# Kernel optimization log

Measured on AMD Instinct MI355X. Metric: run time of the kernel, lower is better.

Reference implementation:

```python
import jax, jax.numpy as jnp
import numpy as np

N, DZ, L, H, MLPH, INC = 256, 256, 256, 512, 2048, 8
CAT_IDX = np.arange(0, 192, 2)                      # 96 categorical token positions (interleaved)
NUM_IDX = np.setdiff1d(np.arange(L), CAT_IDX)       # 160 numerical token positions
CARDS = [4, 16, 128]                                # cardinality per categorical group
GSZ = 32                                            # tokens per categorical group
NUM_CARD = 100                                      # cardinality of quantized numerical params


def setup_inputs() -> dict:
    ks = list(jax.random.split(jax.random.key(0), 24))
    def nrm(shape, s=0.02):
        return jax.random.normal(ks.pop(), shape, jnp.float32) * s
    inp = {}
    inp['z'] = jax.random.normal(ks.pop(), (N, DZ), jnp.float32)
    inp['mlp_w0'] = nrm((DZ, MLPH)); inp['mlp_b0'] = jnp.zeros((MLPH,), jnp.float32)
    inp['mlp_w1'] = nrm((MLPH, MLPH)); inp['mlp_b1'] = jnp.zeros((MLPH,), jnp.float32)
    inp['mlp_w2'] = nrm((MLPH, MLPH)); inp['mlp_b2'] = jnp.zeros((MLPH,), jnp.float32)
    inp['conv_w'] = nrm((H, INC)); inp['conv_b'] = jnp.zeros((H,), jnp.float32)
    for g, card in enumerate(CARDS):
        inp[f'cat_w{g}'] = nrm((H, card)); inp[f'cat_b{g}'] = jnp.zeros((card,), jnp.float32)
    inp['num_w'] = nrm((H, 2)); inp['num_b'] = jnp.zeros((2,), jnp.float32)
    inp['num_target'] = jax.random.uniform(ks.pop(), (N, len(NUM_IDX)), jnp.float32)
    inp['cat_target'] = jax.random.randint(ks.pop(), (N, len(CAT_IDX)), 0, 4, jnp.int32)
    return inp


def reference(z, mlp_w0, mlp_b0, mlp_w1, mlp_b1, mlp_w2, mlp_b2, conv_w, conv_b,
              cat_w0, cat_b0, cat_w1, cat_b1, cat_w2, cat_b2, num_w, num_b,
              num_target, cat_target):
    n = z.shape[0]
    # MLP: fc0 -> act -> fc1 -> act -> fc2
    h = z @ mlp_w0 + mlp_b0
    h = jax.nn.relu(h) @ mlp_w1 + mlp_b1
    h = jax.nn.relu(h) @ mlp_w2 + mlp_b2
    h = h.reshape(n, INC, L)                        # (N, C=8, L)
    # act + 1x1 conv to hidden_size, then transpose -> (N, L, H)
    u = jnp.einsum('ncl,hc->nlh', jax.nn.relu(h), conv_w) + conv_b
    # ---- categorical tokens: gather, per-cardinality heads, CE NLL, argmax sample ----
    hc = u[:, CAT_IDX, :]                           # (N, 96, H)
    heads = [(cat_w0, cat_b0), (cat_w1, cat_b1), (cat_w2, cat_b2)]
    nlls, samps = [], []
    for g, (w, b) in enumerate(heads):
        hg = hc[:, g * GSZ:(g + 1) * GSZ, :]        # (N, 32, H)
        logits = hg @ w + b                         # (N, 32, card)
        logp = jax.nn.log_softmax(logits, axis=-1)
        tg = cat_target[:, g * GSZ:(g + 1) * GSZ]
        nlls.append(-jnp.take_along_axis(logp, tg[..., None], axis=-1)[..., 0])
        samps.append(jnp.argmax(logits, axis=-1))
    cat_nll = jnp.concatenate(nlls, axis=1)         # (N, 96)
    cat_samples = jnp.concatenate(samps, axis=1)    # (N, 96)
    # ---- numerical tokens: gather, 2-param discretized logistic, NLL, mode sample ----
    hn = u[:, NUM_IDX, :]                           # (N, 160, H)
    p = hn @ num_w + num_b                          # (N, 160, 2)
    mu = jax.nn.sigmoid(p[..., 0])
    s = jax.nn.softplus(p[..., 1]) + 1e-4
    hb = 1.0 / (2.0 * (NUM_CARD - 1))               # half bin width
    t = num_target
    cdf_p = jax.nn.sigmoid((t + hb - mu) / s)
    cdf_m = jax.nn.sigmoid((t - hb - mu) / s)
    prob = jnp.where(t < hb, cdf_p, jnp.where(t > 1.0 - hb, 1.0 - cdf_m, cdf_p - cdf_m))
    num_nll = -jnp.log(jnp.maximum(prob, 1e-7))     # (N, 160)
    num_samples = jax.lax.stop_gradient(jnp.round(mu * (NUM_CARD - 1)) / (NUM_CARD - 1))
    # ---- scatter samples back into the preallocated output tensor ----
    u_out = jnp.zeros((n, L, 3), jnp.float32)
    u_out = u_out.at[:, CAT_IDX, 0].set(cat_samples.astype(jnp.float32))
    u_out = u_out.at[:, NUM_IDX, 1].set(num_samples)
    return u_out, cat_nll, num_nll
```

## Files before the change

### kernel.cpp

```cpp
#include <hip/hip_runtime.h>
#include <hip/hip_fp16.h>
#include <math.h>

#define NN   256
#define LL   256
#define HH   512
#define MLPHv 2048
#define INCv 8
#define NCOLS 150

typedef _Float16 f16x8 __attribute__((ext_vector_type(8)));
typedef float    f32x4 __attribute__((ext_vector_type(4)));
typedef unsigned short ushort_t;

__device__ __forceinline__ void split1(float f, ushort_t& h, ushort_t& l)
{
    __half hh = __float2half_rn(f);
    h = __half_as_ushort(hh);
    l = __half_as_ushort(__float2half_rn((f - __half2float(hh)) * 4096.f));
}

__device__ __forceinline__ void pack8(const float* fv, uint4& hv, uint4& lv)
{
    ushort_t h[8], l[8];
#pragma unroll
    for (int j = 0; j < 8; ++j) split1(fv[j], h[j], l[j]);
    hv.x = (unsigned)h[0] | ((unsigned)h[1] << 16);
    hv.y = (unsigned)h[2] | ((unsigned)h[3] << 16);
    hv.z = (unsigned)h[4] | ((unsigned)h[5] << 16);
    hv.w = (unsigned)h[6] | ((unsigned)h[7] << 16);
    lv.x = (unsigned)l[0] | ((unsigned)l[1] << 16);
    lv.y = (unsigned)l[2] | ((unsigned)l[3] << 16);
    lv.z = (unsigned)l[4] | ((unsigned)l[5] << 16);
    lv.w = (unsigned)l[6] | ((unsigned)l[7] << 16);
}

typedef __attribute__((address_space(3))) unsigned int lds_u32;
typedef __attribute__((address_space(1))) const unsigned int glb_u32;
__device__ __forceinline__ void gl_lds16(const ushort_t* g, ushort_t* l)
{
    __builtin_amdgcn_global_load_lds((glb_u32*)g, (lds_u32*)l, 16, 0, 0);
}


__global__ __launch_bounds__(256) void prep_all(
    const float* __restrict__ z,
    const float* __restrict__ w0, const float* __restrict__ w1,
    const float* __restrict__ w2,
    const float* __restrict__ cvw, const float* __restrict__ cvb,
    const float* __restrict__ cw0, const float* __restrict__ cb0,
    const float* __restrict__ cw1, const float* __restrict__ cb1,
    const float* __restrict__ cw2, const float* __restrict__ cb2,
    const float* __restrict__ nw,  const float* __restrict__ nbv,
    ushort_t* __restrict__ W0th, ushort_t* __restrict__ W0tl,
    ushort_t* __restrict__ W1th, ushort_t* __restrict__ W1tl,
    ushort_t* __restrict__ W2th, ushort_t* __restrict__ W2tl,
    ushort_t* __restrict__ zh, ushort_t* __restrict__ zl,
    float* __restrict__ Mf, float* __restrict__ beta)
{
    const int bid = blockIdx.x;
    const int tid = threadIdx.x;
    if (bid < 2176) {
        __shared__ float lfs[64 * 68];
        const float* src; ushort_t* dh; ushort_t* dl; int KS32v, t;
        if (bid < 1024)      { src = w1; dh = W1th; dl = W1tl; KS32v = 64; t = bid; }
        else if (bid < 2048) { src = w2; dh = W2th; dl = W2tl; KS32v = 64; t = bid - 1024; }
        else                 { src = w0; dh = W0th; dl = W0tl; KS32v = 8;  t = bid - 2048; }
        const int k0 = (t >> 5) * 64;
        const int n0 = (t & 31) * 64;
        {
            const int r  = tid >> 2;
            const int cb = (tid & 3) * 16;
            const float* p = src + (size_t)(k0 + r) * 2048 + n0 + cb;
#pragma unroll
            for (int q = 0; q < 4; ++q)
                *(float4*)&lfs[r * 68 + cb + q * 4] = *(const float4*)(p + q * 4);
        }
        __syncthreads();
        {
            const int c  = tid >> 2;
            const int kq = tid & 3;
            ushort_t hb[16], lb[16];
#pragma unroll
            for (int j = 0; j < 16; ++j)
                split1(lfs[(kq * 16 + j) * 68 + c], hb[j], lb[j]);
            const int gn  = (n0 + c) >> 4;
            const int l16 = c & 15;
#pragma unroll
            for (int o = 0; o < 2; ++o) {
                const int koct  = (k0 >> 3) + kq * 2 + o;
                const int ks    = koct >> 2, koct3 = koct & 3;
                const size_t off = ((size_t)(gn * KS32v + ks) * 64 + l16 + (koct3 << 4)) * 8;
                uint4 v;
                v.x = (unsigned)hb[o*8+0] | ((unsigned)hb[o*8+1] << 16);
                v.y = (unsigned)hb[o*8+2] | ((unsigned)hb[o*8+3] << 16);
                v.z = (unsigned)hb[o*8+4] | ((unsigned)hb[o*8+5] << 16);
                v.w = (unsigned)hb[o*8+6] | ((unsigned)hb[o*8+7] << 16);
                *(uint4*)&dh[off] = v;
                v.x = (unsigned)lb[o*8+0] | ((unsigned)lb[o*8+1] << 16);
                v.y = (unsigned)lb[o*8+2] | ((unsigned)lb[o*8+3] << 16);
                v.z = (unsigned)lb[o*8+4] | ((unsigned)lb[o*8+5] << 16);
                v.w = (unsigned)lb[o*8+6] | ((unsigned)lb[o*8+7] << 16);
                *(uint4*)&dl[off] = v;
            }
        }
    } else if (bid < 2192) {
        const int idx = (bid - 2176) * 256 + tid;
        const int r = idx >> 4, kq = idx & 15;
        const float* p = z + (size_t)r * 256 + kq * 16;
        float fv[16];
#pragma unroll
        for (int q = 0; q < 4; ++q) {
            float4 v = *(const float4*)(p + q * 4);
            fv[q * 4 + 0] = v.x; fv[q * 4 + 1] = v.y;
            fv[q * 4 + 2] = v.z; fv[q * 4 + 3] = v.w;
        }
        ushort_t hb[16], lb[16];
#pragma unroll
        for (int j = 0; j < 16; ++j) split1(fv[j], hb[j], lb[j]);
        const int gm = r >> 4, l16 = r & 15;
#pragma unroll
        for (int o = 0; o < 2; ++o) {
            const int koct = kq * 2 + o;
            const int ks = koct >> 2, koct3 = koct & 3;
            const size_t off = ((size_t)(gm * 8 + ks) * 64 + l16 + (koct3 << 4)) * 8;
            uint4 v;
            v.x = (unsigned)hb[o*8+0] | ((unsigned)hb[o*8+1] << 16);
            v.y = (unsigned)hb[o*8+2] | ((unsigned)hb[o*8+3] << 16);
            v.z = (unsigned)hb[o*8+4] | ((unsigned)hb[o*8+5] << 16);
            v.w = (unsigned)hb[o*8+6] | ((unsigned)hb[o*8+7] << 16);
            *(uint4*)&zh[off] = v;
            v.x = (unsigned)lb[o*8+0] | ((unsigned)lb[o*8+1] << 16);
            v.y = (unsigned)lb[o*8+2] | ((unsigned)lb[o*8+3] << 16);
            v.z = (unsigned)lb[o*8+4] | ((unsigned)lb[o*8+5] << 16);
            v.w = (unsigned)lb[o*8+6] | ((unsigned)lb[o*8+7] << 16);
            *(uint4*)&zl[off] = v;
        }
    } else {
        const int k = bid - 2192;
        const float* W; const float* B; int off, card;
        if (k < 4)        { W = cw0; B = cb0; off = 0;   card = 4;   }
        else if (k < 20)  { W = cw1; B = cb1; off = 4;   card = 16;  }
        else if (k < 148) { W = cw2; B = cb2; off = 20;  card = 128; }
        else              { W = nw;  B = nbv; off = 148; card = 2;   }
        const int kc = k - off;
        float part[INCv + 1];
#pragma unroll
        for (int c = 0; c <= INCv; ++c) part[c] = 0.f;
#pragma unroll
        for (int it = 0; it < 2; ++it) {
            const int h = tid + it * 256;
            const float wv = W[h * card + kc];
#pragma unroll
            for (int c = 0; c < INCv; ++c) part[c] += cvw[h * INCv + c] * wv;
            part[INCv] += cvb[h] * wv;
        }
        __shared__ float red[INCv + 1][4];
        const int lane = tid & 63, wave = tid >> 6;
#pragma unroll
        for (int c = 0; c <= INCv; ++c) {
            float v = part[c];
#pragma unroll
            for (int o = 32; o >= 1; o >>= 1) v += __shfl_down(v, o, 64);
            if (lane == 0) red[c][wave] = v;
        }
        __syncthreads();
        if (tid <= INCv) {
            const float s = red[tid][0] + red[tid][1] + red[tid][2] + red[tid][3];
            if (tid < INCv) Mf[tid * NCOLS + k] = s;
            else            beta[k] = s + B[kc];
        }
    }
}

template <int OUT>
__global__ __launch_bounds__(512, 4) void gemm_pk(
    const ushort_t* __restrict__ Ah, const ushort_t* __restrict__ Al,
    const ushort_t* __restrict__ Bh, const ushort_t* __restrict__ Bl,
    const float* __restrict__ bias, float* __restrict__ part,
    ushort_t* __restrict__ oH, ushort_t* __restrict__ oL,
    int KS32, int kchunk32, int steps)
{
    __shared__ ushort_t sAh[2][8192];
    __shared__ ushort_t sAl[2][8192];
    __shared__ ushort_t sBh[2][4096];
    __shared__ ushort_t sBl[2][4096];

    const int tid  = threadIdx.x;
    const int lane = tid & 63, w = tid >> 6;
    const int wr   = w >> 1, wc = w & 1;
    const int bx   = blockIdx.x, by = blockIdx.y, bz = blockIdx.z;
    const int kb0  = bz * kchunk32;

    f32x4 accH[2][2], accC[2][2];
#pragma unroll
    for (int r = 0; r < 2; ++r)
#pragma unroll
        for (int c = 0; c < 2; ++c) {
            accH[r][c] = (f32x4){0.f, 0.f, 0.f, 0.f};
            accC[r][c] = (f32x4){0.f, 0.f, 0.f, 0.f};
        }

    {
        const int kb = kb0;
#pragma unroll
        for (int i = 0; i < 2; ++i) {
            const int run = w + i * 8;
            const int g = run >> 1, ks = run & 1;
            const size_t f = ((size_t)(by * 8 + g) * KS32 + kb + ks) * 512 + lane * 8;
            gl_lds16(Ah + f, &sAh[0][run * 512]);
            gl_lds16(Al + f, &sAl[0][run * 512]);
        }
        const int g = w >> 1, ks = w & 1;
        const size_t f = ((size_t)(bx * 4 + g) * KS32 + kb + ks) * 512 + lane * 8;
        gl_lds16(Bh + f, &sBh[0][w * 512]);
        gl_lds16(Bl + f, &sBl[0][w * 512]);
    }

    for (int t = 0; t < steps; ++t) {
        const int cur = t & 1;
        const int nxt = t + 1;
        if (nxt < steps) {
            const int kb = kb0 + nxt * 2;
            const int nb = nxt & 1;
#pragma unroll
            for (int i = 0; i < 2; ++i) {
                const int run = w + i * 8;
                const int g = run >> 1, ks = run & 1;
                const size_t f = ((size_t)(by * 8 + g) * KS32 + kb + ks) * 512 + lane * 8;
                gl_lds16(Ah + f, &sAh[nb][run * 512]);
                gl_lds16(Al + f, &sAl[nb][run * 512]);
            }
            const int g = w >> 1, ks = w & 1;
            const size_t f = ((size_t)(bx * 4 + g) * KS32 + kb + ks) * 512 + lane * 8;
            gl_lds16(Bh + f, &sBh[nb][w * 512]);
            gl_lds16(Bl + f, &sBl[nb][w * 512]);
            asm volatile("s_waitcnt vmcnt(6)" ::: "memory");
        } else {
            asm volatile("s_waitcnt vmcnt(0)" ::: "memory");
        }
        __builtin_amdgcn_s_barrier();

#pragma unroll
        for (int ks = 0; ks < 2; ++ks) {
            f16x8 aH[2], aL[2], bHf[2], bLf[2];
#pragma unroll
            for (int r = 0; r < 2; ++r) {
                const int off = (((wr * 2 + r) * 2 + ks) * 64 + lane) * 8;
                aH[r] = *(const f16x8*)&sAh[cur][off];
                aL[r] = *(const f16x8*)&sAl[cur][off];
            }
#pragma unroll
            for (int c = 0; c < 2; ++c) {
                const int off = (((wc * 2 + c) * 2 + ks) * 64 + lane) * 8;
                bHf[c] = *(const f16x8*)&sBh[cur][off];
                bLf[c] = *(const f16x8*)&sBl[cur][off];
            }
#pragma unroll
            for (int r = 0; r < 2; ++r)
#pragma unroll
                for (int c = 0; c < 2; ++c) {
                    accH[r][c] = __builtin_amdgcn_mfma_f32_16x16x32_f16(aH[r], bHf[c], accH[r][c], 0, 0, 0);
                    accC[r][c] = __builtin_amdgcn_mfma_f32_16x16x32_f16(aH[r], bLf[c], accC[r][c], 0, 0, 0);
                    accC[r][c] = __builtin_amdgcn_mfma_f32_16x16x32_f16(aL[r], bHf[c], accC[r][c], 0, 0, 0);
                }
        }
        __builtin_amdgcn_s_barrier();
    }

    const float inv = 1.f / 4096.f;
#pragma unroll
    for (int r = 0; r < 2; ++r)
#pragma unroll
        for (int c = 0; c < 2; ++c) {
            const int row0 = by * 128 + (wr * 2 + r) * 16 + ((lane >> 4) << 2);
            const int col  = bx * 64  + (wc * 2 + c) * 16 + (lane & 15);
            if (OUT == 0) {
                float* po = part + (size_t)bz * 524288;
#pragma unroll
                for (int e = 0; e < 4; ++e)
                    po[(size_t)(row0 + e) * 2048 + col] = accH[r][c][e] + accC[r][c][e] * inv;
            } else {
                const float vb = bias[col];
                const int gm = (by * 8 + wr * 2 + r);
                const int ks = col >> 5, koct3 = (col >> 3) & 3, j = col & 7;
                const size_t fb = ((size_t)(gm * 64 + ks) * 64) * 8 + (koct3 << 4) * 8 + j;
#pragma unroll
                for (int e = 0; e < 4; ++e) {
                    const float v = fmaxf(accH[r][c][e] + accC[r][c][e] * inv + vb, 0.f);
                    ushort_t h, l;
                    split1(v, h, l);
                    const int l16 = ((lane >> 4) << 2) + e;
                    oH[fb + (size_t)l16 * 8] = h;
                    oL[fb + (size_t)l16 * 8] = l;
                }
            }
        }
}

__global__ __launch_bounds__(256) void reduce_pk(
    const float* __restrict__ part, const float* __restrict__ bias,
    ushort_t* __restrict__ oH, ushort_t* __restrict__ oL)
{
    const int b  = blockIdx.x;
    const int ct = b & 15, rg = b >> 4;
    const int e  = threadIdx.x * 4;
    const int row = rg * 8 + (e >> 7);
    const int col = ct * 128 + (e & 127);
    const size_t idx = (size_t)row * 2048 + col;
    float4 s = *(const float4*)&bias[col];
#pragma unroll
    for (int k = 0; k < 4; ++k) {
        const float4 p = *(const float4*)&part[(size_t)k * 524288 + idx];
        s.x += p.x; s.y += p.y; s.z += p.z; s.w += p.w;
    }
    s.x = fmaxf(s.x, 0.f); s.y = fmaxf(s.y, 0.f);
    s.z = fmaxf(s.z, 0.f); s.w = fmaxf(s.w, 0.f);
    ushort_t h[4], l[4];
    split1(s.x, h[0], l[0]); split1(s.y, h[1], l[1]);
    split1(s.z, h[2], l[2]); split1(s.w, h[3], l[3]);
    const int gm = row >> 4, l16 = row & 15;
    const int ks = col >> 5, koct3 = (col >> 3) & 3, j = col & 7;
    const size_t off = ((size_t)(gm * 64 + ks) * 64 + l16 + (koct3 << 4)) * 8 + j;
    ushort4 hv = {h[0], h[1], h[2], h[3]};
    ushort4 lv = {l[0], l[1], l[2], l[3]};
    *(ushort4*)&oH[off] = hv;
    *(ushort4*)&oL[off] = lv;
}

__global__ __launch_bounds__(256) void heads_kernel(
    const float* __restrict__ part, const float* __restrict__ b2,
    const float* __restrict__ Mf, const float* __restrict__ beta,
    const int* __restrict__ cat_target, const float* __restrict__ num_target,
    float* __restrict__ out)
{
    const int bx  = blockIdx.x;
    const int tid = threadIdx.x;
    __shared__ float Ms[INCv][128];
    __shared__ float Bsh[128];
    if (bx < 96) {
        const int g = bx >> 5;
        const int card = (g == 0) ? 4 : (g == 1) ? 16 : 128;
        const int off  = (g == 0) ? 0 : (g == 1) ? 4  : 20;
        for (int i = tid; i < card * INCv; i += 256) {
            int c = i / card, k = i % card;
            Ms[c][k] = Mf[c * NCOLS + off + k];
        }
        for (int i = tid; i < card; i += 256) Bsh[i] = beta[off + i];
        __syncthreads();

        const int idx = (bx & 31) * 256 + tid;
        const int n = idx >> 5, j = idx & 31;
        const int ci = g * 32 + j;
        const int l  = ci * 2;
        float rv[INCv];
#pragma unroll
        for (int c = 0; c < INCv; ++c) {
            const size_t e = (size_t)n * MLPHv + c * LL + l;
            float s = b2[c * LL + l];
#pragma unroll
            for (int k = 0; k < 4; ++k) s += part[(size_t)k * 524288 + e];
            rv[c] = fmaxf(s, 0.f);
        }

        float mx = -1e30f; int arg = 0;
        for (int k = 0; k < card; ++k) {
            float s = Bsh[k];
#pragma unroll
            for (int c = 0; c < INCv; ++c) s += rv[c] * Ms[c][k];
            if (s > mx) { mx = s; arg = k; }
        }
        const int tg = cat_target[n * 96 + ci];
        float sum = 0.f, stg = 0.f;
        for (int k = 0; k < card; ++k) {
            float s = Bsh[k];
#pragma unroll
            for (int c = 0; c < INCv; ++c) s += rv[c] * Ms[c][k];
            sum += expf(s - mx);
            if (k == tg) stg = s;
        }
        const float lse = mx + logf(sum);
        out[NN * LL * 3 + n * 96 + ci] = lse - stg;
        float* u = out + (size_t)(n * LL + l) * 3;
        u[0] = (float)arg; u[1] = 0.f; u[2] = 0.f;
    } else {
        const int idx = (bx - 96) * 256 + tid;
        const int n = idx / 160, ni = idx % 160;
        const int l = (ni < 96) ? (2 * ni + 1) : (96 + ni);
        float rv[INCv];
#pragma unroll
        for (int c = 0; c < INCv; ++c) {
            const size_t e = (size_t)n * MLPHv + c * LL + l;
            float s = b2[c * LL + l];
#pragma unroll
            for (int k = 0; k < 4; ++k) s += part[(size_t)k * 524288 + e];
            rv[c] = fmaxf(s, 0.f);
        }
        float p0 = beta[148], p1 = beta[149];
#pragma unroll
        for (int c = 0; c < INCv; ++c) {
            p0 += rv[c] * Mf[c * NCOLS + 148];
            p1 += rv[c] * Mf[c * NCOLS + 149];
        }
        const float mu = 1.f / (1.f + expf(-p0));
        const float sp = (p1 > 20.f) ? p1 : log1pf(expf(p1));
        const float s  = sp + 1e-4f;
        const float hb = 1.f / 198.f;
        const float t  = num_target[n * 160 + ni];
        const float cp = 1.f / (1.f + expf(-((t + hb - mu) / s)));
        const float cm = 1.f / (1.f + expf(-((t - hb - mu) / s)));
        const float prob = (t < hb) ? cp : ((t > 1.f - hb) ? (1.f - cm) : (cp - cm));
        out[NN * LL * 3 + NN * 96 + n * 160 + ni] = -logf(fmaxf(prob, 1e-7f));
        float* u = out + (size_t)(n * LL + l) * 3;
        u[0] = 0.f; u[1] = rintf(mu * 99.f) / 99.f; u[2] = 0.f;
    }
}

extern "C" void kernel_launch(void* const* d_in, const int* in_sizes, int n_in,
                              void* d_out, int out_size, void* d_ws, size_t ws_size,
                              hipStream_t stream)
{
    const float* z   = (const float*)d_in[0];
    const float* w0  = (const float*)d_in[1];
    const float* b0  = (const float*)d_in[2];
    const float* w1  = (const float*)d_in[3];
    const float* b1  = (const float*)d_in[4];
    const float* w2  = (const float*)d_in[5];
    const float* b2  = (const float*)d_in[6];
    const float* cvw = (const float*)d_in[7];
    const float* cvb = (const float*)d_in[8];
    const float* cw0 = (const float*)d_in[9];
    const float* cb0 = (const float*)d_in[10];
    const float* cw1 = (const float*)d_in[11];
    const float* cb1 = (const float*)d_in[12];
    const float* cw2 = (const float*)d_in[13];
    const float* cb2 = (const float*)d_in[14];
    const float* nw  = (const float*)d_in[15];
    const float* nb  = (const float*)d_in[16];
    const float* num_target = (const float*)d_in[17];
    const int*   cat_target = (const int*)d_in[18];
    float* out = (float*)d_out;
    float* ws  = (float*)d_ws;

    size_t o = 0;
    float*    part = ws + o;                o += 4ull * 524288;
    float*    Mf   = ws + o;                o += 1536;
    float*    beta = ws + o;                o += 256;
    ushort_t* zh   = (ushort_t*)(ws + o);   o += 32768;
    ushort_t* zl   = (ushort_t*)(ws + o);   o += 32768;
    ushort_t* r0h  = (ushort_t*)(ws + o);   o += 262144;
    ushort_t* r0l  = (ushort_t*)(ws + o);   o += 262144;
    ushort_t* r1h  = (ushort_t*)(ws + o);   o += 262144;
    ushort_t* r1l  = (ushort_t*)(ws + o);   o += 262144;
    ushort_t* W0th = (ushort_t*)(ws + o);   o += 262144;
    ushort_t* W0tl = (ushort_t*)(ws + o);   o += 262144;
    ushort_t* W1th = (ushort_t*)(ws + o);   o += 2097152;
    ushort_t* W1tl = (ushort_t*)(ws + o);   o += 2097152;
    ushort_t* W2th = (ushort_t*)(ws + o);   o += 2097152;
    ushort_t* W2tl = (ushort_t*)(ws + o);   o += 2097152;

    prep_all<<<dim3(2342), 256, 0, stream>>>(
        z, w0, w1, w2, cvw, cvb, cw0, cb0, cw1, cb1, cw2, cb2, nw, nb,
        W0th, W0tl, W1th, W1tl, W2th, W2tl, zh, zl, Mf, beta);

    gemm_pk<1><<<dim3(32, 2, 1), 512, 0, stream>>>(
        zh, zl, W0th, W0tl, b0, nullptr, r0h, r0l, 8, 8, 4);

    gemm_pk<0><<<dim3(32, 2, 4), 512, 0, stream>>>(
        r0h, r0l, W1th, W1tl, nullptr, part, nullptr, nullptr, 64, 16, 8);
    reduce_pk<<<dim3(512), 256, 0, stream>>>(part, b1, r1h, r1l);

    gemm_pk<0><<<dim3(32, 2, 4), 512, 0, stream>>>(
        r1h, r1l, W2th, W2tl, nullptr, part, nullptr, nullptr, 64, 16, 8);

    heads_kernel<<<dim3(256), 256, 0, stream>>>(
        part, b2, Mf, beta, cat_target, num_target, out);
}
```

Before: 77.81 us.

## Fuse weight fp16 hi/lo split into GEMM tile loads, drop prep pass

Removes the separate prep pass that converted and repacked the full fp32 MLP weights into fp16 hi/lo tiled buffers. Each GEMM block now loads raw fp32 weight tiles into LDS and splits and packs them to fp16 hi/lo in shared memory before the MFMA steps. This saves a full read-convert-write round trip over about 32 MB of weights. In exchange, each weight tile is converted once per M-block (twice here), each step gains an extra barrier, and LDS use grows, so launch bounds drop to one block per SM.

After: 73.73 us. 5.2% less time.

```diff
diff --git a/kernel.cpp b/kernel.cpp
--- a/kernel.cpp
+++ b/kernel.cpp
@@ -41,71 +41,26 @@
 {
     __builtin_amdgcn_global_load_lds((glb_u32*)g, (lds_u32*)l, 16, 0, 0);
 }
-
-
-__global__ __launch_bounds__(256) void prep_all(
+__device__ __forceinline__ void gl_lds16f(const float* g, float* l)
+{
+    __builtin_amdgcn_global_load_lds((glb_u32*)g, (lds_u32*)l, 16, 0, 0);
+}
+
+
+__global__ __launch_bounds__(256) void prep_small(
     const float* __restrict__ z,
-    const float* __restrict__ w0, const float* __restrict__ w1,
-    const float* __restrict__ w2,
     const float* __restrict__ cvw, const float* __restrict__ cvb,
     const float* __restrict__ cw0, const float* __restrict__ cb0,
     const float* __restrict__ cw1, const float* __restrict__ cb1,
     const float* __restrict__ cw2, const float* __restrict__ cb2,
     const float* __restrict__ nw,  const float* __restrict__ nbv,
-    ushort_t* __restrict__ W0th, ushort_t* __restrict__ W0tl,
-    ushort_t* __restrict__ W1th, ushort_t* __restrict__ W1tl,
-    ushort_t* __restrict__ W2th, ushort_t* __restrict__ W2tl,
     ushort_t* __restrict__ zh, ushort_t* __restrict__ zl,
     float* __restrict__ Mf, float* __restrict__ beta)
 {
     const int bid = blockIdx.x;
     const int tid = threadIdx.x;
-    if (bid < 2176) {
-        __shared__ float lfs[64 * 68];
-        const float* src; ushort_t* dh; ushort_t* dl; int KS32v, t;
-        if (bid < 1024)      { src = w1; dh = W1th; dl = W1tl; KS32v = 64; t = bid; }
-        else if (bid < 2048) { src = w2; dh = W2th; dl = W2tl; KS32v = 64; t = bid - 1024; }
-        else                 { src = w0; dh = W0th; dl = W0tl; KS32v = 8;  t = bid - 2048; }
-        const int k0 = (t >> 5) * 64;
-        const int n0 = (t & 31) * 64;
-        {
-            const int r  = tid >> 2;
-            const int cb = (tid & 3) * 16;
-            const float* p = src + (size_t)(k0 + r) * 2048 + n0 + cb;
-#pragma unroll
-            for (int q = 0; q < 4; ++q)
-                *(float4*)&lfs[r * 68 + cb + q * 4] = *(const float4*)(p + q * 4);
-        }
-        __syncthreads();
-        {
-            const int c  = tid >> 2;
-            const int kq = tid & 3;
-            ushort_t hb[16], lb[16];
-#pragma unroll
-            for (int j = 0; j < 16; ++j)
-                split1(lfs[(kq * 16 + j) * 68 + c], hb[j], lb[j]);
-            const int gn  = (n0 + c) >> 4;
-            const int l16 = c & 15;
-#pragma unroll
-            for (int o = 0; o < 2; ++o) {
-                const int koct  = (k0 >> 3) + kq * 2 + o;
-                const int ks    = koct >> 2, koct3 = koct & 3;
-                const size_t off = ((size_t)(gn * KS32v + ks) * 64 + l16 + (koct3 << 4)) * 8;
-                uint4 v;
-                v.x = (unsigned)hb[o*8+0] | ((unsigned)hb[o*8+1] << 16);
-                v.y = (unsigned)hb[o*8+2] | ((unsigned)hb[o*8+3] << 16);
-                v.z = (unsigned)hb[o*8+4] | ((unsigned)hb[o*8+5] << 16);
-                v.w = (unsigned)hb[o*8+6] | ((unsigned)hb[o*8+7] << 16);
-                *(uint4*)&dh[off] = v;
-                v.x = (unsigned)lb[o*8+0] | ((unsigned)lb[o*8+1] << 16);
-                v.y = (unsigned)lb[o*8+2] | ((unsigned)lb[o*8+3] << 16);
-                v.z = (unsigned)lb[o*8+4] | ((unsigned)lb[o*8+5] << 16);
-                v.w = (unsigned)lb[o*8+6] | ((unsigned)lb[o*8+7] << 16);
-                *(uint4*)&dl[off] = v;
-            }
-        }
-    } else if (bid < 2192) {
-        const int idx = (bid - 2176) * 256 + tid;
+    if (bid < 16) {
+        const int idx = bid * 256 + tid;
         const int r = idx >> 4, kq = idx & 15;
         const float* p = z + (size_t)r * 256 + kq * 16;
         float fv[16];
@@ -115,29 +70,19 @@
             fv[q * 4 + 0] = v.x; fv[q * 4 + 1] = v.y;
             fv[q * 4 + 2] = v.z; fv[q * 4 + 3] = v.w;
         }
-        ushort_t hb[16], lb[16];
-#pragma unroll
-        for (int j = 0; j < 16; ++j) split1(fv[j], hb[j], lb[j]);
         const int gm = r >> 4, l16 = r & 15;
 #pragma unroll
         for (int o = 0; o < 2; ++o) {
+            uint4 hv, lv;
+            pack8(&fv[o * 8], hv, lv);
             const int koct = kq * 2 + o;
             const int ks = koct >> 2, koct3 = koct & 3;
             const size_t off = ((size_t)(gm * 8 + ks) * 64 + l16 + (koct3 << 4)) * 8;
-            uint4 v;
-            v.x = (unsigned)hb[o*8+0] | ((unsigned)hb[o*8+1] << 16);
-            v.y = (unsigned)hb[o*8+2] | ((unsigned)hb[o*8+3] << 16);
-            v.z = (unsigned)hb[o*8+4] | ((unsigned)hb[o*8+5] << 16);
-            v.w = (unsigned)hb[o*8+6] | ((unsigned)hb[o*8+7] << 16);
-            *(uint4*)&zh[off] = v;
-            v.x = (unsigned)lb[o*8+0] | ((unsigned)lb[o*8+1] << 16);
-            v.y = (unsigned)lb[o*8+2] | ((unsigned)lb[o*8+3] << 16);
-            v.z = (unsigned)lb[o*8+4] | ((unsigned)lb[o*8+5] << 16);
-            v.w = (unsigned)lb[o*8+6] | ((unsigned)lb[o*8+7] << 16);
-            *(uint4*)&zl[off] = v;
+            *(uint4*)&zh[off] = hv;
+            *(uint4*)&zl[off] = lv;
         }
     } else {
-        const int k = bid - 2192;
+        const int k = bid - 16;
         const float* W; const float* B; int off, card;
         if (k < 4)        { W = cw0; B = cb0; off = 0;   card = 4;   }
         else if (k < 20)  { W = cw1; B = cb1; off = 4;   card = 16;  }
@@ -174,22 +119,23 @@
 }
 
 template <int OUT>
-__global__ __launch_bounds__(512, 4) void gemm_pk(
+__global__ __launch_bounds__(512, 1) void gemm_wf(
     const ushort_t* __restrict__ Ah, const ushort_t* __restrict__ Al,
-    const ushort_t* __restrict__ Bh, const ushort_t* __restrict__ Bl,
-    const float* __restrict__ bias, float* __restrict__ part,
-    ushort_t* __restrict__ oH, ushort_t* __restrict__ oL,
+    const float* __restrict__ W, const float* __restrict__ bias,
+    float* __restrict__ part, ushort_t* __restrict__ oH, ushort_t* __restrict__ oL,
     int KS32, int kchunk32, int steps)
 {
     __shared__ ushort_t sAh[2][8192];
     __shared__ ushort_t sAl[2][8192];
-    __shared__ ushort_t sBh[2][4096];
-    __shared__ ushort_t sBl[2][4096];
+    __shared__ float    sWf[2][4160];
+    __shared__ ushort_t sWh[2][4096];
+    __shared__ ushort_t sWl[2][4096];
 
     const int tid  = threadIdx.x;
     const int lane = tid & 63, w = tid >> 6;
     const int wr   = w >> 1, wc = w & 1;
     const int bx   = blockIdx.x, by = blockIdx.y, bz = blockIdx.z;
+    const int bn   = bx * 64;
     const int kb0  = bz * kchunk32;
 
     f32x4 accH[2][2], accC[2][2];
@@ -201,45 +147,56 @@
             accC[r][c] = (f32x4){0.f, 0.f, 0.f, 0.f};
         }
 
-    {
-        const int kb = kb0;
+    auto STAGE = [&](int ts, int b) {
+        const int kb = kb0 + ts * 2;
 #pragma unroll
         for (int i = 0; i < 2; ++i) {
             const int run = w + i * 8;
             const int g = run >> 1, ks = run & 1;
             const size_t f = ((size_t)(by * 8 + g) * KS32 + kb + ks) * 512 + lane * 8;
-            gl_lds16(Ah + f, &sAh[0][run * 512]);
-            gl_lds16(Al + f, &sAl[0][run * 512]);
-        }
-        const int g = w >> 1, ks = w & 1;
-        const size_t f = ((size_t)(bx * 4 + g) * KS32 + kb + ks) * 512 + lane * 8;
-        gl_lds16(Bh + f, &sBh[0][w * 512]);
-        gl_lds16(Bl + f, &sBl[0][w * 512]);
-    }
-
+            gl_lds16(Ah + f, &sAh[b][run * 512]);
+            gl_lds16(Al + f, &sAl[b][run * 512]);
+        }
+        const int k0 = kb * 32;
+#pragma unroll
+        for (int ii = 0; ii < 2; ++ii) {
+            const int i = w * 2 + ii;
+            const float* src = W + (size_t)(k0 + i * 4 + (lane >> 4)) * 2048 + bn + (lane & 15) * 4;
+            gl_lds16f(src, &sWf[b][i * 260]);
+        }
+    };
+
+    STAGE(0, 0);
     for (int t = 0; t < steps; ++t) {
         const int cur = t & 1;
-        const int nxt = t + 1;
-        if (nxt < steps) {
-            const int kb = kb0 + nxt * 2;
-            const int nb = nxt & 1;
-#pragma unroll
-            for (int i = 0; i < 2; ++i) {
-                const int run = w + i * 8;
-                const int g = run >> 1, ks = run & 1;
-                const size_t f = ((size_t)(by * 8 + g) * KS32 + kb + ks) * 512 + lane * 8;
-                gl_lds16(Ah + f, &sAh[nb][run * 512]);
-                gl_lds16(Al + f, &sAl[nb][run * 512]);
-            }
-            const int g = w >> 1, ks = w & 1;
-            const size_t f = ((size_t)(bx * 4 + g) * KS32 + kb + ks) * 512 + lane * 8;
-            gl_lds16(Bh + f, &sBh[nb][w * 512]);
-            gl_lds16(Bl + f, &sBl[nb][w * 512]);
+        if (t + 1 < steps) {
+            STAGE(t + 1, cur ^ 1);
             asm volatile("s_waitcnt vmcnt(6)" ::: "memory");
         } else {
             asm volatile("s_waitcnt vmcnt(0)" ::: "memory");
         }
         __builtin_amdgcn_s_barrier();
+        asm volatile("" ::: "memory");
+
+        {
+            const int col = lane;
+            const int i0  = w * 2;
+            float fv[8];
+#pragma unroll
+            for (int j = 0; j < 4; ++j) fv[j]     = sWf[cur][i0 * 260 + j * 64 + col];
+#pragma unroll
+            for (int j = 0; j < 4; ++j) fv[4 + j] = sWf[cur][(i0 + 1) * 260 + j * 64 + col];
+            uint4 hv, lv;
+            pack8(fv, hv, lv);
+            const int g = col >> 4, l16 = col & 15;
+            const int ks = w >> 2, koct = w & 3;
+            const int ub = ((g * 2 + ks) * 64 + l16 + koct * 16) * 8;
+            *(uint4*)&sWh[cur][ub] = hv;
+            *(uint4*)&sWl[cur][ub] = lv;
+        }
+        asm volatile("s_waitcnt lgkmcnt(0)" ::: "memory");
+        __builtin_amdgcn_s_barrier();
+        asm volatile("" ::: "memory");
 
 #pragma unroll
         for (int ks = 0; ks < 2; ++ks) {
@@ -253,8 +210,8 @@
 #pragma unroll
             for (int c = 0; c < 2; ++c) {
                 const int off = (((wc * 2 + c) * 2 + ks) * 64 + lane) * 8;
-                bHf[c] = *(const f16x8*)&sBh[cur][off];
-                bLf[c] = *(const f16x8*)&sBl[cur][off];
+                bHf[c] = *(const f16x8*)&sWh[cur][off];
+                bLf[c] = *(const f16x8*)&sWl[cur][off];
             }
 #pragma unroll
             for (int r = 0; r < 2; ++r)
@@ -266,6 +223,7 @@
                 }
         }
         __builtin_amdgcn_s_barrier();
+        asm volatile("" ::: "memory");
     }
 
     const float inv = 1.f / 4096.f;
@@ -274,7 +232,7 @@
 #pragma unroll
         for (int c = 0; c < 2; ++c) {
             const int row0 = by * 128 + (wr * 2 + r) * 16 + ((lane >> 4) << 2);
-            const int col  = bx * 64  + (wc * 2 + c) * 16 + (lane & 15);
+            const int col  = bn + (wc * 2 + c) * 16 + (lane & 15);
             if (OUT == 0) {
                 float* po = part + (size_t)bz * 524288;
 #pragma unroll
@@ -452,26 +410,19 @@
     ushort_t* r0l  = (ushort_t*)(ws + o);   o += 262144;
     ushort_t* r1h  = (ushort_t*)(ws + o);   o += 262144;
     ushort_t* r1l  = (ushort_t*)(ws + o);   o += 262144;
-    ushort_t* W0th = (ushort_t*)(ws + o);   o += 262144;
-    ushort_t* W0tl = (ushort_t*)(ws + o);   o += 262144;
-    ushort_t* W1th = (ushort_t*)(ws + o);   o += 2097152;
-    ushort_t* W1tl = (ushort_t*)(ws + o);   o += 2097152;
-    ushort_t* W2th = (ushort_t*)(ws + o);   o += 2097152;
-    ushort_t* W2tl = (ushort_t*)(ws + o);   o += 2097152;
-
-    prep_all<<<dim3(2342), 256, 0, stream>>>(
-        z, w0, w1, w2, cvw, cvb, cw0, cb0, cw1, cb1, cw2, cb2, nw, nb,
-        W0th, W0tl, W1th, W1tl, W2th, W2tl, zh, zl, Mf, beta);
-
-    gemm_pk<1><<<dim3(32, 2, 1), 512, 0, stream>>>(
-        zh, zl, W0th, W0tl, b0, nullptr, r0h, r0l, 8, 8, 4);
-
-    gemm_pk<0><<<dim3(32, 2, 4), 512, 0, stream>>>(
-        r0h, r0l, W1th, W1tl, nullptr, part, nullptr, nullptr, 64, 16, 8);
+
+    prep_small<<<dim3(166), 256, 0, stream>>>(
+        z, cvw, cvb, cw0, cb0, cw1, cb1, cw2, cb2, nw, nb, zh, zl, Mf, beta);
+
+    gemm_wf<1><<<dim3(32, 2, 1), 512, 0, stream>>>(
+        zh, zl, w0, b0, nullptr, r0h, r0l, 8, 8, 4);
+
+    gemm_wf<0><<<dim3(32, 2, 4), 512, 0, stream>>>(
+        r0h, r0l, w1, nullptr, part, nullptr, nullptr, 64, 16, 8);
     reduce_pk<<<dim3(512), 256, 0, stream>>>(part, b1, r1h, r1l);
 
-    gemm_pk<0><<<dim3(32, 2, 4), 512, 0, stream>>>(
-        r1h, r1l, W2th, W2tl, nullptr, part, nullptr, nullptr, 64, 16, 8);
+    gemm_wf<0><<<dim3(32, 2, 4), 512, 0, stream>>>(
+        r1h, r1l, w2, nullptr, part, nullptr, nullptr, 64, 16, 8);
 
     heads_kernel<<<dim3(256), 256, 0, stream>>>(
         part, b2, Mf, beta, cat_target, num_target, out);
```
